# Kernel optimization log

Hardware: AMD Instinct MI355X
Metric: run time of the kernel (lower is better)

The kernel has to match this reference:

```python
import jax, jax.numpy as jnp
import numpy as np

ALPHA = 0.25
GAMMA = 2.0
CLS_EPS = 1e-4


def _make_boxes(key, n, img=512.0, smin=32.0, smax=128.0, yx=False):
    k1, k2, k3, k4 = jax.random.split(key, 4)
    cx = jax.random.uniform(k1, (n,)) * img
    cy = jax.random.uniform(k2, (n,)) * img
    w = smin + jax.random.uniform(k3, (n,)) * (smax - smin)
    h = smin + jax.random.uniform(k4, (n,)) * (smax - smin)
    if yx:  # anchor format (y1, x1, y2, x2)
        return jnp.stack([cy - h / 2, cx - w / 2, cy + h / 2, cx + w / 2], axis=1)
    # annotation format (x1, y1, x2, y2)
    return jnp.stack([cx - w / 2, cy - h / 2, cx + w / 2, cy + h / 2], axis=1)


def setup_inputs() -> dict:
    key = jax.random.key(0)
    B, A, C, M = 4, 100000, 80, 32
    k = jax.random.split(key, 6)
    classifications = jax.random.uniform(k[0], (B, A, C), dtype=jnp.float32)
    regressions = jax.random.normal(k[1], (B, A, 7), dtype=jnp.float32)
    anchors = _make_boxes(k[2], A, yx=True)[None]  # [1, A, 4] (y1,x1,y2,x2)
    boxes = jax.vmap(lambda kk: _make_boxes(kk, M))(jax.random.split(k[3], B))  # [B, M, 4]
    labels = jax.random.randint(k[4], (B, M), 0, C).astype(jnp.float32)
    annotations = jnp.concatenate([boxes, labels[..., None]], axis=-1)  # [B, M, 5]
    return {"classifications": classifications, "regressions": regressions,
            "anchors": anchors, "annotations": annotations}


def reference(classifications, regressions, anchors, annotations):
    B, A, C = classifications.shape
    anchor = anchors[0]  # [A, 4] (y1, x1, y2, x2)
    aw = anchor[:, 3] - anchor[:, 1]
    ah = anchor[:, 2] - anchor[:, 0]
    acx = anchor[:, 1] + 0.5 * aw
    acy = anchor[:, 0] + 0.5 * ah
    area_a = (anchor[:, 2] - anchor[:, 0]) * (anchor[:, 3] - anchor[:, 1])

    def per_image(cls, reg, ann):
        M_ = ann.shape[0]
        b = ann[:, :4]  # (x1, y1, x2, y2)
        labels = ann[:, 4].astype(jnp.int32)
        cls = jnp.clip(cls, CLS_EPS, 1.0 - CLS_EPS)
        # IoU [A, M] (same axis convention as calc_iou)
        iw = jnp.clip(jnp.minimum(anchor[:, 3:4], b[None, :, 2]) - jnp.maximum(anchor[:, 1:2], b[None, :, 0]), 0.0)
        ih = jnp.clip(jnp.minimum(anchor[:, 2:3], b[None, :, 3]) - jnp.maximum(anchor[:, 0:1], b[None, :, 1]), 0.0)
        area_b = (b[:, 2] - b[:, 0]) * (b[:, 3] - b[:, 1])
        inter = iw * ih
        ua = jnp.clip(area_a[:, None] + area_b[None, :] - inter, 1e-8)
        iou = inter / ua
        iou_max = iou.max(axis=1)
        iou_argmax = iou.argmax(axis=1)  # [A]
        pos = iou_max >= 0.5
        neg = iou_max < 0.4
        num_pos = pos.sum()
        posf = pos.astype(cls.dtype)
        # classification targets: -1 ignore, 0 background, one-hot positives
        assigned_box = b[iou_argmax]           # [A, 4]
        assigned_lbl = labels[iou_argmax]      # [A]
        onehot = jax.nn.one_hot(assigned_lbl, C, dtype=cls.dtype)
        tgt = jnp.where(pos[:, None], onehot, jnp.where(neg[:, None], 0.0, -1.0))
        alpha_f = jnp.where(tgt == 1.0, ALPHA, 1.0 - ALPHA)
        focal_w = alpha_f * jnp.where(tgt == 1.0, 1.0 - cls, cls) ** GAMMA
        bce = -(tgt * jnp.log(cls) + (1.0 - tgt) * jnp.log(1.0 - cls))
        cls_loss = jnp.where(tgt != -1.0, focal_w * bce, 0.0).sum() / jnp.maximum(num_pos.astype(cls.dtype), 1.0)
        gw = assigned_box[:, 2] - assigned_box[:, 0]
        gh = assigned_box[:, 3] - assigned_box[:, 1]
        gcx = assigned_box[:, 0] + 0.5 * gw
        gcy = assigned_box[:, 1] + 0.5 * gh
        gw = jnp.clip(gw, 1.0)
        gh = jnp.clip(gh, 1.0)
        rt = jnp.stack([(gcy - acy) / ah, (gcx - acx) / aw,
                        jnp.log(gh / ah), jnp.log(gw / aw)], axis=1)  # [A, 4] (dy,dx,dh,dw)
        diff = jnp.abs(rt - reg[:, :4])
        sl1 = jnp.where(diff <= 1.0 / 9.0, 0.5 * 9.0 * diff ** 2, diff - 0.5 / 9.0)
        reg_loss = (sl1 * posf[:, None]).sum() / jnp.maximum(num_pos * 4, 1).astype(cls.dtype)
        # embedding grouping loss (segment mean per GT box over positive anchors)
        emb = reg[:, 4:7]
        counts = jax.ops.segment_sum(posf, iou_argmax, num_segments=M_)          # [M]
        sums = jax.ops.segment_sum(emb * posf[:, None], iou_argmax, num_segments=M_)  # [M, 3]
        mean = jnp.where((counts > 0)[:, None], sums / jnp.maximum(counts, 1.0)[:, None], 0.0)
        mdet = jax.lax.stop_gradient(mean)
        sq = jax.ops.segment_sum((((emb - mdet[iou_argmax]) ** 2).sum(-1)) * posf, iou_argmax, num_segments=M_)
        per_ann = jnp.where(counts > 0, sq / jnp.maximum(counts * 3.0, 1.0), 0.0)
        emb_loss = per_ann.sum() / M_
        return cls_loss, reg_loss, emb_loss, mean

    cls_l, reg_l, emb_l, embs = jax.vmap(per_image)(classifications, regressions, annotations)
    losses = jnp.stack([cls_l.mean(), reg_l.mean() * 50.0, emb_l.mean()])
    return losses, embs
```

## Files before the change

kernel.cpp:

```cpp
#include <hip/hip_runtime.h>

#define CLS_LO 1.0e-4f
#define CLS_HI 0.9999f


__device__ __forceinline__ float smooth_l1(float d) {
    d = fabsf(d);
    return (d <= (1.0f / 9.0f)) ? (4.5f * d * d) : (d - (0.5f / 9.0f));
}

__global__ void __launch_bounds__(256)
det_assign_kernel(const float* __restrict__ cls,
                  const float* __restrict__ reg,
                  const float* __restrict__ anc,
                  const float* __restrict__ ann,
                  float* __restrict__ ws,
                  float* __restrict__ maskf,
                  int A, int C, int M)
{
    const int b   = blockIdx.y;
    const int tid = threadIdx.x;
    const int a   = blockIdx.x * 256 + tid;
    const int S   = 5 * M + 192;

    __shared__ float4 sbox[64];
    __shared__ float  slbl[64];
    __shared__ float  s_cnt[64], s_sx[64], s_sy[64], s_sz[64], s_sq[64];
    __shared__ float  s_part[4][3];

    if (tid < M) {
        const float* bp = ann + ((size_t)b * M + tid) * 5;
        sbox[tid] = make_float4(bp[0], bp[1], bp[2], bp[3]);
        slbl[tid] = bp[4];
        s_cnt[tid] = 0.f; s_sx[tid] = 0.f; s_sy[tid] = 0.f; s_sz[tid] = 0.f; s_sq[tid] = 0.f;
    }
    __syncthreads();

    float contrib_cls = 0.f, contrib_reg = 0.f, contrib_np = 0.f;

    if (a < A) {
        float4 av = ((const float4*)anc)[a];
        const float ay1 = av.x, ax1 = av.y, ay2 = av.z, ax2 = av.w;
        const float aw  = ax2 - ax1;
        const float ah  = ay2 - ay1;
        const float area_a = ah * aw;

        float bN = -1.f, bD = 1.f;
        int   bj = 0;
#define IOU_BODY(j)                                                              \
        {                                                                        \
            const float4 bx = sbox[(j)];                                         \
            float iw = fminf(ax2, bx.z) - fmaxf(ax1, bx.x); iw = fmaxf(iw, 0.f); \
            float ih = fminf(ay2, bx.w) - fmaxf(ay1, bx.y); ih = fmaxf(ih, 0.f); \
            const float inter = iw * ih;                                         \
            const float ua = fmaxf(area_a + (bx.z - bx.x) * (bx.w - bx.y)        \
                                   - inter, 1e-8f);                              \
            if (inter * bD > bN * ua) { bN = inter; bD = ua; bj = (j); }         \
        }
        if (M == 32) {
            #pragma unroll
            for (int j = 0; j < 32; j++) IOU_BODY(j)
        } else {
            for (int j = 0; j < M; j++) IOU_BODY(j)
        }
#undef IOU_BODY
        const bool pos = (2.f * bN >= bD);
        const bool neg = (bN < 0.4f * bD);
        maskf[(size_t)b * A + a] = (pos || neg) ? 1.f : 0.f;

        if (pos) {
            contrib_np = 1.0f;

            const float* cbase = cls + ((size_t)b * A + a) * (size_t)C;
            const int L = (int)slbl[bj];
            const float p = fminf(fmaxf(cbase[L], CLS_LO), CLS_HI);
            contrib_cls = 0.25f * (1.f - p) * (1.f - p) * (-__logf(p))
                        - 0.75f * p * p * (-__logf(1.f - p));

            const float* rp = reg + ((size_t)b * A + a) * 7;
            const float r0 = rp[0], r1 = rp[1], r2 = rp[2], r3 = rp[3];
            const float e0 = rp[4], e1 = rp[5], e2 = rp[6];

            const float4 bx = sbox[bj];
            float gw = bx.z - bx.x;
            float gh = bx.w - bx.y;
            const float gcx = bx.x + 0.5f * gw;
            const float gcy = bx.y + 0.5f * gh;
            gw = fmaxf(gw, 1.f);
            gh = fmaxf(gh, 1.f);
            const float acx = ax1 + 0.5f * aw;
            const float acy = ay1 + 0.5f * ah;
            contrib_reg = smooth_l1((gcy - acy) / ah - r0) +
                          smooth_l1((gcx - acx) / aw - r1) +
                          smooth_l1(__logf(gh / ah) - r2) +
                          smooth_l1(__logf(gw / aw) - r3);

            atomicAdd(&s_cnt[bj], 1.f);
            atomicAdd(&s_sx[bj], e0);
            atomicAdd(&s_sy[bj], e1);
            atomicAdd(&s_sz[bj], e2);
            atomicAdd(&s_sq[bj], e0 * e0 + e1 * e1 + e2 * e2);
        }
    }

    for (int off = 32; off > 0; off >>= 1) {
        contrib_cls += __shfl_down(contrib_cls, off, 64);
        contrib_reg += __shfl_down(contrib_reg, off, 64);
        contrib_np  += __shfl_down(contrib_np,  off, 64);
    }
    if ((tid & 63) == 0) {
        s_part[tid >> 6][0] = contrib_cls;
        s_part[tid >> 6][1] = contrib_reg;
        s_part[tid >> 6][2] = contrib_np;
    }
    __syncthreads();

    float* wsb = ws + (size_t)b * S;
    if (tid < M) {
        const float c = s_cnt[tid];
        if (c != 0.f) {
            atomicAdd(&wsb[tid], c);
            atomicAdd(&wsb[M + 3 * tid + 0], s_sx[tid]);
            atomicAdd(&wsb[M + 3 * tid + 1], s_sy[tid]);
            atomicAdd(&wsb[M + 3 * tid + 2], s_sz[tid]);
            atomicAdd(&wsb[4 * M + tid], s_sq[tid]);
        }
    }
    if (tid == 0) {
        const float c = s_part[0][0] + s_part[1][0] + s_part[2][0] + s_part[3][0];
        const float r = s_part[0][1] + s_part[1][1] + s_part[2][1] + s_part[3][1];
        const float n = s_part[0][2] + s_part[1][2] + s_part[2][2] + s_part[3][2];
        float* slot = wsb + 5 * M + 3 * (blockIdx.x & 63);
        if (c != 0.f) atomicAdd(&slot[0], c);
        if (r != 0.f) atomicAdd(&slot[1], r);
        if (n != 0.f) atomicAdd(&slot[2], n);
    }
}

typedef const __attribute__((address_space(1))) unsigned int ga_u32;
typedef __attribute__((address_space(3))) unsigned int ls_u32;

template <int CPA4>
__global__ void __launch_bounds__(256)
det_focal_kernel(const float* __restrict__ cls,
                 const float* __restrict__ maskf,
                 float* __restrict__ ws,
                 int A, int C, int M)
{
    const int b     = blockIdx.y;
    const int aBase = blockIdx.x * 64;
    const int tid   = threadIdx.x;
    const int S     = 5 * M + 192;
    const int cpa4  = CPA4 ? CPA4 : (C >> 2);

    __shared__ float tile[64 * 80];
    __shared__ float smask[64];

    const int nA = min(64, A - aBase);
    const float* gtile = cls + ((size_t)b * A + aBase) * (size_t)C;
    float acc = 0.f;

    if (CPA4 == 20 && nA == 64) {
        const int wave = tid >> 6;
        const int lane = tid & 63;
        #pragma unroll
        for (int k = 0; k < 5; k++) {
            const int f4 = wave * 320 + k * 64 + lane;
            const float* g = gtile + 4 * f4;
            float* l = tile + 4 * (wave * 320 + k * 64);
            __builtin_amdgcn_global_load_lds((ga_u32*)g, (ls_u32*)l, 16, 0, 0);
        }
        if (tid < 64) smask[tid] = maskf[(size_t)b * A + aBase + tid];
        __builtin_amdgcn_s_waitcnt(0);
        __syncthreads();

        #pragma unroll
        for (int k = 0; k < 5; k++) {
            const unsigned idx = (unsigned)tid + 256u * k;
            const float4 v = ((const float4*)tile)[idx];
            const float m = smask[(idx * 52429u) >> 20];
            float p, l, s = 0.f;
            p = fminf(fmaxf(v.x, CLS_LO), CLS_HI); l = __logf(1.f - p); s = fmaf(p * p, l, s);
            p = fminf(fmaxf(v.y, CLS_LO), CLS_HI); l = __logf(1.f - p); s = fmaf(p * p, l, s);
            p = fminf(fmaxf(v.z, CLS_LO), CLS_HI); l = __logf(1.f - p); s = fmaf(p * p, l, s);
            p = fminf(fmaxf(v.w, CLS_LO), CLS_HI); l = __logf(1.f - p); s = fmaf(p * p, l, s);
            acc = fmaf(m, s, acc);
        }
    } else {
        if (tid < 64) smask[tid] = (aBase + tid < A) ? maskf[(size_t)b * A + aBase + tid] : 0.f;
        __syncthreads();
        const int n4 = nA * cpa4;
        for (int idx = tid; idx < n4; idx += 256) {
            const float m = smask[(unsigned)idx / (unsigned)cpa4];
            const float4 vv = ((const float4*)gtile)[idx];
            float p, l, s = 0.f;
            p = fminf(fmaxf(vv.x, CLS_LO), CLS_HI); l = __logf(1.f - p); s = fmaf(p * p, l, s);
            p = fminf(fmaxf(vv.y, CLS_LO), CLS_HI); l = __logf(1.f - p); s = fmaf(p * p, l, s);
            p = fminf(fmaxf(vv.z, CLS_LO), CLS_HI); l = __logf(1.f - p); s = fmaf(p * p, l, s);
            p = fminf(fmaxf(vv.w, CLS_LO), CLS_HI); l = __logf(1.f - p); s = fmaf(p * p, l, s);
            acc = fmaf(m, s, acc);
        }
    }

    for (int off = 32; off > 0; off >>= 1)
        acc += __shfl_down(acc, off, 64);
    __shared__ float sp[4];
    if ((tid & 63) == 0) sp[tid >> 6] = acc;
    __syncthreads();
    if (tid == 0) {
        const float tot = sp[0] + sp[1] + sp[2] + sp[3];
        atomicAdd(&ws[(size_t)b * S + 5 * M + 3 * (blockIdx.x & 63) + 0], -0.75f * tot);
    }
}

__global__ void __launch_bounds__(256)
det_final_kernel(const float* __restrict__ ws,
                 float* __restrict__ out,
                 int B, int M)
{
    const int t = threadIdx.x;
    const int S = 5 * M + 192;
    __shared__ float s_scal[8][3];
    __shared__ float s_emb[8];
    if (t < B) s_emb[t] = 0.f;

    const int k = t & 63;
    for (int b = t >> 6; b < B; b += 4) {
        const float* slot = ws + (size_t)b * S + 5 * M + 3 * k;
        float c = slot[0], r = slot[1], n = slot[2];
        for (int off = 32; off > 0; off >>= 1) {
            c += __shfl_down(c, off, 64);
            r += __shfl_down(r, off, 64);
            n += __shfl_down(n, off, 64);
        }
        if (k == 0) { s_scal[b][0] = c; s_scal[b][1] = r; s_scal[b][2] = n; }
    }
    __syncthreads();

    if (t < B * M) {
        const int b = t / M;
        const int m = t - b * M;
        const float* wsb = ws + (size_t)b * S;
        const float c = wsb[m];
        float mx = 0.f, my = 0.f, mz = 0.f, pa = 0.f;
        if (c > 0.f) {
            mx = wsb[M + 3 * m + 0] / c;
            my = wsb[M + 3 * m + 1] / c;
            mz = wsb[M + 3 * m + 2] / c;
            const float sq = wsb[4 * M + m] - c * (mx * mx + my * my + mz * mz);
            pa = sq / fmaxf(c * 3.f, 1.f);
        }
        out[3 + (size_t)(b * M + m) * 3 + 0] = mx;
        out[3 + (size_t)(b * M + m) * 3 + 1] = my;
        out[3 + (size_t)(b * M + m) * 3 + 2] = mz;
        atomicAdd(&s_emb[b], pa);
    }
    __syncthreads();

    if (t == 0) {
        float cl = 0.f, rl = 0.f, el = 0.f;
        for (int b = 0; b < B; b++) {
            const float np = s_scal[b][2];
            cl += s_scal[b][0] / fmaxf(np, 1.f);
            rl += s_scal[b][1] / fmaxf(4.f * np, 1.f);
            el += s_emb[b] / (float)M;
        }
        const float invB = 1.f / (float)B;
        out[0] = cl * invB;
        out[1] = rl * invB * 50.f;
        out[2] = el * invB;
    }
}

extern "C" void kernel_launch(void* const* d_in, const int* in_sizes, int n_in,
                              void* d_out, int out_size, void* d_ws, size_t ws_size,
                              hipStream_t stream) {
    const float* cls = (const float*)d_in[0];
    const float* reg = (const float*)d_in[1];
    const float* anc = (const float*)d_in[2];
    const float* ann = (const float*)d_in[3];
    float* out = (float*)d_out;
    float* ws  = (float*)d_ws;

    const int A = in_sizes[2] / 4;
    const int B = in_sizes[1] / (A * 7);
    const int C = in_sizes[0] / (B * A);
    const int M = in_sizes[3] / (B * 5);
    const int S = 5 * M + 192;
    float* maskf = ws + (size_t)B * S;

    hipMemsetAsync(ws, 0, (size_t)B * S * sizeof(float), stream);

    dim3 gridA((A + 255) / 256, B);
    det_assign_kernel<<<gridA, 256, 0, stream>>>(cls, reg, anc, ann, ws, maskf, A, C, M);

    dim3 gridB((A + 63) / 64, B);
    if (C == 80)
        det_focal_kernel<20><<<gridB, 256, 0, stream>>>(cls, maskf, ws, A, C, M);
    else
        det_focal_kernel<0><<<gridB, 256, 0, stream>>>(cls, maskf, ws, A, C, M);

    det_final_kernel<<<1, 256, 0, stream>>>(ws, out, B, M);
}
```

Measured before the change: 241.3 us.

## Fuse assignment, focal-loss and final reduction into one kernel with last-block finish

Merges the anchor-assignment kernel, the dense focal-loss pass and the final reduction into a single kernel. Each block now keeps its positive/negative mask in shared memory instead of writing it to global memory and reading it back. The last block to finish, found through an atomic counter, does the final reduction, which removes two kernel launches. Per-block partial sums are stored to slots rather than accumulated with atomics. The trade-off is a larger per-block working set and the loss of the global_load_lds staging path for the 80-class case.

```diff
diff --git a/kernel.cpp b/kernel.cpp
--- a/kernel.cpp
+++ b/kernel.cpp
@@ -9,24 +9,40 @@
     return (d <= (1.0f / 9.0f)) ? (4.5f * d * d) : (d - (0.5f / 9.0f));
 }
 
+__device__ __forceinline__ float aload(const float* p) {
+    return __hip_atomic_load(p, __ATOMIC_RELAXED, __HIP_MEMORY_SCOPE_AGENT);
+}
+__device__ __forceinline__ void astore(float* p, float v) {
+    __hip_atomic_store(p, v, __ATOMIC_RELAXED, __HIP_MEMORY_SCOPE_AGENT);
+}
+
+template <int CPA4>
 __global__ void __launch_bounds__(256)
-det_assign_kernel(const float* __restrict__ cls,
-                  const float* __restrict__ reg,
-                  const float* __restrict__ anc,
-                  const float* __restrict__ ann,
-                  float* __restrict__ ws,
-                  float* __restrict__ maskf,
-                  int A, int C, int M)
+det_fused_kernel(const float* __restrict__ cls,
+                 const float* __restrict__ reg,
+                 const float* __restrict__ anc,
+                 const float* __restrict__ ann,
+                 float* __restrict__ ws,
+                 float* __restrict__ out,
+                 int A, int C, int M, int B, int NBx)
 {
-    const int b   = blockIdx.y;
+    const int gid = blockIdx.x;
+    const int b   = gid / NBx;
+    const int bx  = gid - b * NBx;
     const int tid = threadIdx.x;
-    const int a   = blockIdx.x * 256 + tid;
-    const int S   = 5 * M + 192;
+    const int a0  = bx * 256;
+    const int a   = a0 + tid;
+    const int cpa4 = CPA4 ? CPA4 : (C >> 2);
+
+    unsigned int* done = (unsigned int*)(ws + (size_t)B * 5 * M);
+    float* slots = ws + (size_t)B * 5 * M + 4;
 
     __shared__ float4 sbox[64];
     __shared__ float  slbl[64];
     __shared__ float  s_cnt[64], s_sx[64], s_sy[64], s_sz[64], s_sq[64];
+    __shared__ float  smask[256];
     __shared__ float  s_part[4][3];
+    __shared__ bool   s_last;
 
     if (tid < M) {
         const float* bp = ann + ((size_t)b * M + tid) * 5;
@@ -34,6 +50,7 @@
         slbl[tid] = bp[4];
         s_cnt[tid] = 0.f; s_sx[tid] = 0.f; s_sy[tid] = 0.f; s_sz[tid] = 0.f; s_sq[tid] = 0.f;
     }
+    smask[tid] = 0.f;
     __syncthreads();
 
     float contrib_cls = 0.f, contrib_reg = 0.f, contrib_np = 0.f;
@@ -49,11 +66,11 @@
         int   bj = 0;
 #define IOU_BODY(j)                                                              \
         {                                                                        \
-            const float4 bx = sbox[(j)];                                         \
-            float iw = fminf(ax2, bx.z) - fmaxf(ax1, bx.x); iw = fmaxf(iw, 0.f); \
-            float ih = fminf(ay2, bx.w) - fmaxf(ay1, bx.y); ih = fmaxf(ih, 0.f); \
+            const float4 bx4 = sbox[(j)];                                        \
+            float iw = fminf(ax2, bx4.z) - fmaxf(ax1, bx4.x); iw = fmaxf(iw, 0.f);\
+            float ih = fminf(ay2, bx4.w) - fmaxf(ay1, bx4.y); ih = fmaxf(ih, 0.f);\
             const float inter = iw * ih;                                         \
-            const float ua = fmaxf(area_a + (bx.z - bx.x) * (bx.w - bx.y)        \
+            const float ua = fmaxf(area_a + (bx4.z - bx4.x) * (bx4.w - bx4.y)    \
                                    - inter, 1e-8f);                              \
             if (inter * bD > bN * ua) { bN = inter; bD = ua; bj = (j); }         \
         }
@@ -66,7 +83,7 @@
 #undef IOU_BODY
         const bool pos = (2.f * bN >= bD);
         const bool neg = (bN < 0.4f * bD);
-        maskf[(size_t)b * A + a] = (pos || neg) ? 1.f : 0.f;
+        smask[tid] = (pos || neg) ? 1.f : 0.f;
 
         if (pos) {
             contrib_np = 1.0f;
@@ -81,11 +98,11 @@
             const float r0 = rp[0], r1 = rp[1], r2 = rp[2], r3 = rp[3];
             const float e0 = rp[4], e1 = rp[5], e2 = rp[6];
 
-            const float4 bx = sbox[bj];
-            float gw = bx.z - bx.x;
-            float gh = bx.w - bx.y;
-            const float gcx = bx.x + 0.5f * gw;
-            const float gcy = bx.y + 0.5f * gh;
+            const float4 bx4 = sbox[bj];
+            float gw = bx4.z - bx4.x;
+            float gh = bx4.w - bx4.y;
+            const float gcx = bx4.x + 0.5f * gw;
+            const float gcy = bx4.y + 0.5f * gh;
             gw = fmaxf(gw, 1.f);
             gh = fmaxf(gh, 1.f);
             const float acx = ax1 + 0.5f * aw;
@@ -102,6 +119,49 @@
             atomicAdd(&s_sq[bj], e0 * e0 + e1 * e1 + e2 * e2);
         }
     }
+    __syncthreads();
+
+    {
+        const int nA = min(256, A - a0);
+        const float4* tile = (const float4*)(cls + ((size_t)b * A + a0) * (size_t)C);
+        float acc = 0.f;
+
+        if (CPA4 == 20 && nA == 256) {
+            #pragma unroll
+            for (int g = 0; g < 4; g++) {
+                float4 v[5];
+                float  mk[5];
+                #pragma unroll
+                for (int k = 0; k < 5; k++)
+                    v[k] = tile[tid + 256 * (g * 5 + k)];
+                #pragma unroll
+                for (int k = 0; k < 5; k++)
+                    mk[k] = smask[(((unsigned)tid + 256u * (g * 5 + k)) * 52429u) >> 20];
+                #pragma unroll
+                for (int k = 0; k < 5; k++) {
+                    float p, l, s = 0.f;
+                    p = fminf(fmaxf(v[k].x, CLS_LO), CLS_HI); l = __logf(1.f - p); s = fmaf(p * p, l, s);
+                    p = fminf(fmaxf(v[k].y, CLS_LO), CLS_HI); l = __logf(1.f - p); s = fmaf(p * p, l, s);
+                    p = fminf(fmaxf(v[k].z, CLS_LO), CLS_HI); l = __logf(1.f - p); s = fmaf(p * p, l, s);
+                    p = fminf(fmaxf(v[k].w, CLS_LO), CLS_HI); l = __logf(1.f - p); s = fmaf(p * p, l, s);
+                    acc = fmaf(mk[k], s, acc);
+                }
+            }
+        } else if (nA > 0) {
+            const int n4 = nA * cpa4;
+            for (int idx = tid; idx < n4; idx += 256) {
+                const float m = smask[(unsigned)idx / (unsigned)cpa4];
+                const float4 vv = tile[idx];
+                float p, l, s = 0.f;
+                p = fminf(fmaxf(vv.x, CLS_LO), CLS_HI); l = __logf(1.f - p); s = fmaf(p * p, l, s);
+                p = fminf(fmaxf(vv.y, CLS_LO), CLS_HI); l = __logf(1.f - p); s = fmaf(p * p, l, s);
+                p = fminf(fmaxf(vv.z, CLS_LO), CLS_HI); l = __logf(1.f - p); s = fmaf(p * p, l, s);
+                p = fminf(fmaxf(vv.w, CLS_LO), CLS_HI); l = __logf(1.f - p); s = fmaf(p * p, l, s);
+                acc = fmaf(m, s, acc);
+            }
+        }
+        contrib_cls -= 0.75f * acc;
+    }
 
     for (int off = 32; off > 0; off >>= 1) {
         contrib_cls += __shfl_down(contrib_cls, off, 64);
@@ -115,7 +175,7 @@
     }
     __syncthreads();
 
-    float* wsb = ws + (size_t)b * S;
+    float* wsb = ws + (size_t)b * 5 * M;
     if (tid < M) {
         const float c = s_cnt[tid];
         if (c != 0.f) {
@@ -127,143 +187,73 @@
         }
     }
     if (tid == 0) {
-        const float c = s_part[0][0] + s_part[1][0] + s_part[2][0] + s_part[3][0];
-        const float r = s_part[0][1] + s_part[1][1] + s_part[2][1] + s_part[3][1];
-        const float n = s_part[0][2] + s_part[1][2] + s_part[2][2] + s_part[3][2];
-        float* slot = wsb + 5 * M + 3 * (blockIdx.x & 63);
-        if (c != 0.f) atomicAdd(&slot[0], c);
-        if (r != 0.f) atomicAdd(&slot[1], r);
-        if (n != 0.f) atomicAdd(&slot[2], n);
-    }
-}
-
-typedef const __attribute__((address_space(1))) unsigned int ga_u32;
-typedef __attribute__((address_space(3))) unsigned int ls_u32;
-
-template <int CPA4>
-__global__ void __launch_bounds__(256)
-det_focal_kernel(const float* __restrict__ cls,
-                 const float* __restrict__ maskf,
-                 float* __restrict__ ws,
-                 int A, int C, int M)
-{
-    const int b     = blockIdx.y;
-    const int aBase = blockIdx.x * 64;
-    const int tid   = threadIdx.x;
-    const int S     = 5 * M + 192;
-    const int cpa4  = CPA4 ? CPA4 : (C >> 2);
-
-    __shared__ float tile[64 * 80];
-    __shared__ float smask[64];
-
-    const int nA = min(64, A - aBase);
-    const float* gtile = cls + ((size_t)b * A + aBase) * (size_t)C;
-    float acc = 0.f;
-
-    if (CPA4 == 20 && nA == 64) {
-        const int wave = tid >> 6;
-        const int lane = tid & 63;
-        #pragma unroll
-        for (int k = 0; k < 5; k++) {
-            const int f4 = wave * 320 + k * 64 + lane;
-            const float* g = gtile + 4 * f4;
-            float* l = tile + 4 * (wave * 320 + k * 64);
-            __builtin_amdgcn_global_load_lds((ga_u32*)g, (ls_u32*)l, 16, 0, 0);
-        }
-        if (tid < 64) smask[tid] = maskf[(size_t)b * A + aBase + tid];
-        __builtin_amdgcn_s_waitcnt(0);
-        __syncthreads();
-
-        #pragma unroll
-        for (int k = 0; k < 5; k++) {
-            const unsigned idx = (unsigned)tid + 256u * k;
-            const float4 v = ((const float4*)tile)[idx];
-            const float m = smask[(idx * 52429u) >> 20];
-            float p, l, s = 0.f;
-            p = fminf(fmaxf(v.x, CLS_LO), CLS_HI); l = __logf(1.f - p); s = fmaf(p * p, l, s);
-            p = fminf(fmaxf(v.y, CLS_LO), CLS_HI); l = __logf(1.f - p); s = fmaf(p * p, l, s);
-            p = fminf(fmaxf(v.z, CLS_LO), CLS_HI); l = __logf(1.f - p); s = fmaf(p * p, l, s);
-            p = fminf(fmaxf(v.w, CLS_LO), CLS_HI); l = __logf(1.f - p); s = fmaf(p * p, l, s);
-            acc = fmaf(m, s, acc);
-        }
-    } else {
-        if (tid < 64) smask[tid] = (aBase + tid < A) ? maskf[(size_t)b * A + aBase + tid] : 0.f;
-        __syncthreads();
-        const int n4 = nA * cpa4;
-        for (int idx = tid; idx < n4; idx += 256) {
-            const float m = smask[(unsigned)idx / (unsigned)cpa4];
-            const float4 vv = ((const float4*)gtile)[idx];
-            float p, l, s = 0.f;
-            p = fminf(fmaxf(vv.x, CLS_LO), CLS_HI); l = __logf(1.f - p); s = fmaf(p * p, l, s);
-            p = fminf(fmaxf(vv.y, CLS_LO), CLS_HI); l = __logf(1.f - p); s = fmaf(p * p, l, s);
-            p = fminf(fmaxf(vv.z, CLS_LO), CLS_HI); l = __logf(1.f - p); s = fmaf(p * p, l, s);
-            p = fminf(fmaxf(vv.w, CLS_LO), CLS_HI); l = __logf(1.f - p); s = fmaf(p * p, l, s);
-            acc = fmaf(m, s, acc);
-        }
-    }
-
-    for (int off = 32; off > 0; off >>= 1)
-        acc += __shfl_down(acc, off, 64);
-    __shared__ float sp[4];
-    if ((tid & 63) == 0) sp[tid >> 6] = acc;
-    __syncthreads();
-    if (tid == 0) {
-        const float tot = sp[0] + sp[1] + sp[2] + sp[3];
-        atomicAdd(&ws[(size_t)b * S + 5 * M + 3 * (blockIdx.x & 63) + 0], -0.75f * tot);
-    }
-}
-
-__global__ void __launch_bounds__(256)
-det_final_kernel(const float* __restrict__ ws,
-                 float* __restrict__ out,
-                 int B, int M)
-{
-    const int t = threadIdx.x;
-    const int S = 5 * M + 192;
+        float* slot = slots + 3 * (size_t)gid;
+        astore(&slot[0], s_part[0][0] + s_part[1][0] + s_part[2][0] + s_part[3][0]);
+        astore(&slot[1], s_part[0][1] + s_part[1][1] + s_part[2][1] + s_part[3][1]);
+        astore(&slot[2], s_part[0][2] + s_part[1][2] + s_part[2][2] + s_part[3][2]);
+        __threadfence();
+        const unsigned old = atomicAdd(done, 1u);
+        s_last = (old == (unsigned)(B * NBx - 1));
+    }
+    __syncthreads();
+    if (!s_last) return;
+
+    __threadfence();
     __shared__ float s_scal[8][3];
     __shared__ float s_emb[8];
-    if (t < B) s_emb[t] = 0.f;
-
-    const int k = t & 63;
-    for (int b = t >> 6; b < B; b += 4) {
-        const float* slot = ws + (size_t)b * S + 5 * M + 3 * k;
-        float c = slot[0], r = slot[1], n = slot[2];
+    __shared__ float tmp[4][3];
+    if (tid < B) s_emb[tid] = 0.f;
+
+    for (int bb = 0; bb < B; bb++) {
+        float c = 0.f, r = 0.f, n = 0.f;
+        for (int i = tid; i < NBx; i += 256) {
+            const float* slot = slots + 3 * (size_t)(bb * NBx + i);
+            c += aload(&slot[0]);
+            r += aload(&slot[1]);
+            n += aload(&slot[2]);
+        }
         for (int off = 32; off > 0; off >>= 1) {
             c += __shfl_down(c, off, 64);
             r += __shfl_down(r, off, 64);
             n += __shfl_down(n, off, 64);
         }
-        if (k == 0) { s_scal[b][0] = c; s_scal[b][1] = r; s_scal[b][2] = n; }
-    }
-    __syncthreads();
-
-    if (t < B * M) {
-        const int b = t / M;
-        const int m = t - b * M;
-        const float* wsb = ws + (size_t)b * S;
-        const float c = wsb[m];
+        if ((tid & 63) == 0) { tmp[tid >> 6][0] = c; tmp[tid >> 6][1] = r; tmp[tid >> 6][2] = n; }
+        __syncthreads();
+        if (tid == 0) {
+            s_scal[bb][0] = tmp[0][0] + tmp[1][0] + tmp[2][0] + tmp[3][0];
+            s_scal[bb][1] = tmp[0][1] + tmp[1][1] + tmp[2][1] + tmp[3][1];
+            s_scal[bb][2] = tmp[0][2] + tmp[1][2] + tmp[2][2] + tmp[3][2];
+        }
+        __syncthreads();
+    }
+
+    if (tid < B * M) {
+        const int bb = tid / M;
+        const int m  = tid - bb * M;
+        const float* sg = ws + (size_t)bb * 5 * M;
+        const float c = aload(&sg[m]);
         float mx = 0.f, my = 0.f, mz = 0.f, pa = 0.f;
         if (c > 0.f) {
-            mx = wsb[M + 3 * m + 0] / c;
-            my = wsb[M + 3 * m + 1] / c;
-            mz = wsb[M + 3 * m + 2] / c;
-            const float sq = wsb[4 * M + m] - c * (mx * mx + my * my + mz * mz);
+            mx = aload(&sg[M + 3 * m + 0]) / c;
+            my = aload(&sg[M + 3 * m + 1]) / c;
+            mz = aload(&sg[M + 3 * m + 2]) / c;
+            const float sq = aload(&sg[4 * M + m]) - c * (mx * mx + my * my + mz * mz);
             pa = sq / fmaxf(c * 3.f, 1.f);
         }
-        out[3 + (size_t)(b * M + m) * 3 + 0] = mx;
-        out[3 + (size_t)(b * M + m) * 3 + 1] = my;
-        out[3 + (size_t)(b * M + m) * 3 + 2] = mz;
-        atomicAdd(&s_emb[b], pa);
-    }
-    __syncthreads();
-
-    if (t == 0) {
+        out[3 + (size_t)(bb * M + m) * 3 + 0] = mx;
+        out[3 + (size_t)(bb * M + m) * 3 + 1] = my;
+        out[3 + (size_t)(bb * M + m) * 3 + 2] = mz;
+        atomicAdd(&s_emb[bb], pa);
+    }
+    __syncthreads();
+
+    if (tid == 0) {
         float cl = 0.f, rl = 0.f, el = 0.f;
-        for (int b = 0; b < B; b++) {
-            const float np = s_scal[b][2];
-            cl += s_scal[b][0] / fmaxf(np, 1.f);
-            rl += s_scal[b][1] / fmaxf(4.f * np, 1.f);
-            el += s_emb[b] / (float)M;
+        for (int bb = 0; bb < B; bb++) {
+            const float np = s_scal[bb][2];
+            cl += s_scal[bb][0] / fmaxf(np, 1.f);
+            rl += s_scal[bb][1] / fmaxf(4.f * np, 1.f);
+            el += s_emb[bb] / (float)M;
         }
         const float invB = 1.f / (float)B;
         out[0] = cl * invB;
@@ -286,19 +276,13 @@
     const int B = in_sizes[1] / (A * 7);
     const int C = in_sizes[0] / (B * A);
     const int M = in_sizes[3] / (B * 5);
-    const int S = 5 * M + 192;
-    float* maskf = ws + (size_t)B * S;
-
-    hipMemsetAsync(ws, 0, (size_t)B * S * sizeof(float), stream);
-
-    dim3 gridA((A + 255) / 256, B);
-    det_assign_kernel<<<gridA, 256, 0, stream>>>(cls, reg, anc, ann, ws, maskf, A, C, M);
-
-    dim3 gridB((A + 63) / 64, B);
+    const int NBx = (A + 255) / 256;
+
+    hipMemsetAsync(ws, 0, ((size_t)B * 5 * M + 4) * sizeof(float), stream);
+
+    dim3 grid(B * NBx);
     if (C == 80)
-        det_focal_kernel<20><<<gridB, 256, 0, stream>>>(cls, maskf, ws, A, C, M);
+        det_fused_kernel<20><<<grid, 256, 0, stream>>>(cls, reg, anc, ann, ws, out, A, C, M, B, NBx);
     else
-        det_focal_kernel<0><<<gridB, 256, 0, stream>>>(cls, maskf, ws, A, C, M);
-
-    det_final_kernel<<<1, 256, 0, stream>>>(ws, out, B, M);
-}
+        det_fused_kernel<0><<<grid, 256, 0, stream>>>(cls, reg, anc, ann, ws, out, A, C, M, B, NBx);
+}
```

New measurement: 279.6 us. 15.9% more time.

## Drop mask buffer: sum all negatives unmasked, correct ignored anchors in assign

Applied to the files above, without the earlier changes.

The focal kernel no longer reads a per-anchor mask. It sums the negative-class focal term over every class of every anchor with plain coalesced float4 loads, eight per thread. The assign kernel adds back the term for ignored anchors (neither positive nor negative) by re-reading their class rows, so the mask write and read and the LDS staging go away. This relies on ignored anchors being rare, because each such thread does a strided 80-float row read. Launch bounds now also request 4 blocks per CU.

```diff
diff --git a/kernel.cpp b/kernel.cpp
--- a/kernel.cpp
+++ b/kernel.cpp
@@ -9,13 +9,13 @@
     return (d <= (1.0f / 9.0f)) ? (4.5f * d * d) : (d - (0.5f / 9.0f));
 }
 
-__global__ void __launch_bounds__(256)
+template <int CPA4>
+__global__ void __launch_bounds__(256, 4)
 det_assign_kernel(const float* __restrict__ cls,
                   const float* __restrict__ reg,
                   const float* __restrict__ anc,
                   const float* __restrict__ ann,
                   float* __restrict__ ws,
-                  float* __restrict__ maskf,
                   int A, int C, int M)
 {
     const int b   = blockIdx.y;
@@ -47,15 +47,15 @@
 
         float bN = -1.f, bD = 1.f;
         int   bj = 0;
-#define IOU_BODY(j)                                                              \
-        {                                                                        \
-            const float4 bx = sbox[(j)];                                         \
-            float iw = fminf(ax2, bx.z) - fmaxf(ax1, bx.x); iw = fmaxf(iw, 0.f); \
-            float ih = fminf(ay2, bx.w) - fmaxf(ay1, bx.y); ih = fmaxf(ih, 0.f); \
-            const float inter = iw * ih;                                         \
-            const float ua = fmaxf(area_a + (bx.z - bx.x) * (bx.w - bx.y)        \
-                                   - inter, 1e-8f);                              \
-            if (inter * bD > bN * ua) { bN = inter; bD = ua; bj = (j); }         \
+#define IOU_BODY(j)                                                               \
+        {                                                                         \
+            const float4 bx4 = sbox[(j)];                                         \
+            float iw = fminf(ax2, bx4.z) - fmaxf(ax1, bx4.x); iw = fmaxf(iw, 0.f);\
+            float ih = fminf(ay2, bx4.w) - fmaxf(ay1, bx4.y); ih = fmaxf(ih, 0.f);\
+            const float inter = iw * ih;                                          \
+            const float ua = fmaxf(area_a + (bx4.z - bx4.x) * (bx4.w - bx4.y)     \
+                                   - inter, 1e-8f);                               \
+            if (inter * bD > bN * ua) { bN = inter; bD = ua; bj = (j); }          \
         }
         if (M == 32) {
             #pragma unroll
@@ -66,7 +66,6 @@
 #undef IOU_BODY
         const bool pos = (2.f * bN >= bD);
         const bool neg = (bN < 0.4f * bD);
-        maskf[(size_t)b * A + a] = (pos || neg) ? 1.f : 0.f;
 
         if (pos) {
             contrib_np = 1.0f;
@@ -81,11 +80,11 @@
             const float r0 = rp[0], r1 = rp[1], r2 = rp[2], r3 = rp[3];
             const float e0 = rp[4], e1 = rp[5], e2 = rp[6];
 
-            const float4 bx = sbox[bj];
-            float gw = bx.z - bx.x;
-            float gh = bx.w - bx.y;
-            const float gcx = bx.x + 0.5f * gw;
-            const float gcy = bx.y + 0.5f * gh;
+            const float4 bx4 = sbox[bj];
+            float gw = bx4.z - bx4.x;
+            float gh = bx4.w - bx4.y;
+            const float gcx = bx4.x + 0.5f * gw;
+            const float gcy = bx4.y + 0.5f * gh;
             gw = fmaxf(gw, 1.f);
             gh = fmaxf(gh, 1.f);
             const float acx = ax1 + 0.5f * aw;
@@ -100,6 +99,27 @@
             atomicAdd(&s_sy[bj], e1);
             atomicAdd(&s_sz[bj], e2);
             atomicAdd(&s_sq[bj], e0 * e0 + e1 * e1 + e2 * e2);
+        } else if (!neg) {
+            const float* rowp = cls + ((size_t)b * A + a) * (size_t)C;
+            float s = 0.f;
+            if (CPA4 == 20) {
+                const float4* r4 = (const float4*)rowp;
+                #pragma unroll 5
+                for (int k = 0; k < 20; k++) {
+                    const float4 v = r4[k];
+                    float p;
+                    p = fminf(fmaxf(v.x, CLS_LO), CLS_HI); s = fmaf(p * p, __logf(1.f - p), s);
+                    p = fminf(fmaxf(v.y, CLS_LO), CLS_HI); s = fmaf(p * p, __logf(1.f - p), s);
+                    p = fminf(fmaxf(v.z, CLS_LO), CLS_HI); s = fmaf(p * p, __logf(1.f - p), s);
+                    p = fminf(fmaxf(v.w, CLS_LO), CLS_HI); s = fmaf(p * p, __logf(1.f - p), s);
+                }
+            } else {
+                for (int c = 0; c < C; c++) {
+                    const float p = fminf(fmaxf(rowp[c], CLS_LO), CLS_HI);
+                    s = fmaf(p * p, __logf(1.f - p), s);
+                }
+            }
+            contrib_cls = 0.75f * s;
         }
     }
 
@@ -137,68 +157,50 @@
     }
 }
 
-typedef const __attribute__((address_space(1))) unsigned int ga_u32;
-typedef __attribute__((address_space(3))) unsigned int ls_u32;
-
-template <int CPA4>
-__global__ void __launch_bounds__(256)
+template <bool FAST>
+__global__ void __launch_bounds__(256, 4)
 det_focal_kernel(const float* __restrict__ cls,
-                 const float* __restrict__ maskf,
                  float* __restrict__ ws,
-                 int A, int C, int M)
+                 int A, int C, int M, int N4 )
 {
-    const int b     = blockIdx.y;
-    const int aBase = blockIdx.x * 64;
-    const int tid   = threadIdx.x;
-    const int S     = 5 * M + 192;
-    const int cpa4  = CPA4 ? CPA4 : (C >> 2);
-
-    __shared__ float tile[64 * 80];
-    __shared__ float smask[64];
-
-    const int nA = min(64, A - aBase);
-    const float* gtile = cls + ((size_t)b * A + aBase) * (size_t)C;
+    const int b   = blockIdx.y;
+    const int tid = threadIdx.x;
+    const int S   = 5 * M + 192;
     float acc = 0.f;
 
-    if (CPA4 == 20 && nA == 64) {
-        const int wave = tid >> 6;
-        const int lane = tid & 63;
-        #pragma unroll
-        for (int k = 0; k < 5; k++) {
-            const int f4 = wave * 320 + k * 64 + lane;
-            const float* g = gtile + 4 * f4;
-            float* l = tile + 4 * (wave * 320 + k * 64);
-            __builtin_amdgcn_global_load_lds((ga_u32*)g, (ls_u32*)l, 16, 0, 0);
-        }
-        if (tid < 64) smask[tid] = maskf[(size_t)b * A + aBase + tid];
-        __builtin_amdgcn_s_waitcnt(0);
-        __syncthreads();
-
-        #pragma unroll
-        for (int k = 0; k < 5; k++) {
-            const unsigned idx = (unsigned)tid + 256u * k;
-            const float4 v = ((const float4*)tile)[idx];
-            const float m = smask[(idx * 52429u) >> 20];
-            float p, l, s = 0.f;
-            p = fminf(fmaxf(v.x, CLS_LO), CLS_HI); l = __logf(1.f - p); s = fmaf(p * p, l, s);
-            p = fminf(fmaxf(v.y, CLS_LO), CLS_HI); l = __logf(1.f - p); s = fmaf(p * p, l, s);
-            p = fminf(fmaxf(v.z, CLS_LO), CLS_HI); l = __logf(1.f - p); s = fmaf(p * p, l, s);
-            p = fminf(fmaxf(v.w, CLS_LO), CLS_HI); l = __logf(1.f - p); s = fmaf(p * p, l, s);
-            acc = fmaf(m, s, acc);
+    if (FAST) {
+        const float4* img = (const float4*)(cls + (size_t)b * A * (size_t)C);
+        const int base = blockIdx.x * 2048;
+        if (base + 2048 <= N4) {
+            float4 v[8];
+            #pragma unroll
+            for (int k = 0; k < 8; k++)
+                v[k] = img[base + tid + 256 * k];
+            #pragma unroll
+            for (int k = 0; k < 8; k++) {
+                float p;
+                p = fminf(fmaxf(v[k].x, CLS_LO), CLS_HI); acc = fmaf(p * p, __logf(1.f - p), acc);
+                p = fminf(fmaxf(v[k].y, CLS_LO), CLS_HI); acc = fmaf(p * p, __logf(1.f - p), acc);
+                p = fminf(fmaxf(v[k].z, CLS_LO), CLS_HI); acc = fmaf(p * p, __logf(1.f - p), acc);
+                p = fminf(fmaxf(v[k].w, CLS_LO), CLS_HI); acc = fmaf(p * p, __logf(1.f - p), acc);
+            }
+        } else {
+            for (int idx = base + tid; idx < N4; idx += 256) {
+                const float4 v = img[idx];
+                float p;
+                p = fminf(fmaxf(v.x, CLS_LO), CLS_HI); acc = fmaf(p * p, __logf(1.f - p), acc);
+                p = fminf(fmaxf(v.y, CLS_LO), CLS_HI); acc = fmaf(p * p, __logf(1.f - p), acc);
+                p = fminf(fmaxf(v.z, CLS_LO), CLS_HI); acc = fmaf(p * p, __logf(1.f - p), acc);
+                p = fminf(fmaxf(v.w, CLS_LO), CLS_HI); acc = fmaf(p * p, __logf(1.f - p), acc);
+            }
         }
     } else {
-        if (tid < 64) smask[tid] = (aBase + tid < A) ? maskf[(size_t)b * A + aBase + tid] : 0.f;
-        __syncthreads();
-        const int n4 = nA * cpa4;
-        for (int idx = tid; idx < n4; idx += 256) {
-            const float m = smask[(unsigned)idx / (unsigned)cpa4];
-            const float4 vv = ((const float4*)gtile)[idx];
-            float p, l, s = 0.f;
-            p = fminf(fmaxf(vv.x, CLS_LO), CLS_HI); l = __logf(1.f - p); s = fmaf(p * p, l, s);
-            p = fminf(fmaxf(vv.y, CLS_LO), CLS_HI); l = __logf(1.f - p); s = fmaf(p * p, l, s);
-            p = fminf(fmaxf(vv.z, CLS_LO), CLS_HI); l = __logf(1.f - p); s = fmaf(p * p, l, s);
-            p = fminf(fmaxf(vv.w, CLS_LO), CLS_HI); l = __logf(1.f - p); s = fmaf(p * p, l, s);
-            acc = fmaf(m, s, acc);
+        const float* img = cls + (size_t)b * A * (size_t)C;
+        const int n = A * C;
+        const int stride = gridDim.x * 256;
+        for (int i = blockIdx.x * 256 + tid; i < n; i += stride) {
+            const float p = fminf(fmaxf(img[i], CLS_LO), CLS_HI);
+            acc = fmaf(p * p, __logf(1.f - p), acc);
         }
     }
 
@@ -287,18 +289,24 @@
     const int C = in_sizes[0] / (B * A);
     const int M = in_sizes[3] / (B * 5);
     const int S = 5 * M + 192;
-    float* maskf = ws + (size_t)B * S;
 
     hipMemsetAsync(ws, 0, (size_t)B * S * sizeof(float), stream);
 
     dim3 gridA((A + 255) / 256, B);
-    det_assign_kernel<<<gridA, 256, 0, stream>>>(cls, reg, anc, ann, ws, maskf, A, C, M);
-
-    dim3 gridB((A + 63) / 64, B);
     if (C == 80)
-        det_focal_kernel<20><<<gridB, 256, 0, stream>>>(cls, maskf, ws, A, C, M);
+        det_assign_kernel<20><<<gridA, 256, 0, stream>>>(cls, reg, anc, ann, ws, A, C, M);
     else
-        det_focal_kernel<0><<<gridB, 256, 0, stream>>>(cls, maskf, ws, A, C, M);
+        det_assign_kernel<0><<<gridA, 256, 0, stream>>>(cls, reg, anc, ann, ws, A, C, M);
+
+    if ((C & 3) == 0) {
+        const int N4 = A * (C >> 2);
+        dim3 gridF((N4 + 2047) / 2048, B);
+        det_focal_kernel<true><<<gridF, 256, 0, stream>>>(cls, ws, A, C, M, N4);
+    } else {
+        const int n = A * C;
+        dim3 gridF((n + 8191) / 8192, B);
+        det_focal_kernel<false><<<gridF, 256, 0, stream>>>(cls, ws, A, C, M, 0);
+    }
 
     det_final_kernel<<<1, 256, 0, stream>>>(ws, out, B, M);
 }
```

After: 252.0 us. 4.5% more time.
